# Optimization experiments

Hardware: AMD Instinct MI355X
Metric: run time of the kernel (lower is better)

The kernel has to match this reference:

```python
import jax, jax.numpy as jnp
import numpy as np
from jax import lax

EPS = 1e-5
H = 4      # num_heads
D = 64     # qkv_dim (== in_channels)


def _bn(x, gamma, beta, mean, var):
    # eval-mode BatchNorm2d over NCHW, channel axis 1
    inv = gamma / jnp.sqrt(var + EPS)
    return x * inv[:, None, None] + (beta - mean * inv)[:, None, None]


def _conv(x, w, b, pad_w):
    y = lax.conv_general_dilated(x, w, window_strides=(1, 1),
                                 padding=[(0, 0), (pad_w, pad_w)],
                                 dimension_numbers=("NCHW", "OIHW", "NCHW"))
    return y + b[None, :, None, None]


def setup_inputs() -> dict:
    key = jax.random.key(0)
    ks = jax.random.split(key, 16)
    N, C, T, V = 16, 64, 64, 25
    s = 0.05
    return {
        "x": jax.random.normal(ks[0], (N, C, T, V), jnp.float32),
        "W_qkv": jax.random.normal(ks[1], (C, 3 * H * D), jnp.float32) * s,
        "b_qkv": jax.random.normal(ks[2], (3 * H * D,), jnp.float32) * s,
        "W_out": jax.random.normal(ks[3], (C, C * H, 1, 9), jnp.float32) * s,
        "b_out": jax.random.normal(ks[4], (C,), jnp.float32) * s,
        "bn1_gamma": jax.random.uniform(ks[5], (C,), jnp.float32) + 0.5,
        "bn1_beta": jax.random.normal(ks[6], (C,), jnp.float32) * s,
        "bn1_mean": jax.random.normal(ks[7], (C,), jnp.float32) * s,
        "bn1_var": jax.random.uniform(ks[8], (C,), jnp.float32) + 0.5,
        "W_ff": jax.random.normal(ks[9], (C, C, 1, 1), jnp.float32) * s,
        "b_ff": jax.random.normal(ks[10], (C,), jnp.float32) * s,
        "bn2_gamma": jax.random.uniform(ks[11], (C,), jnp.float32) + 0.5,
        "bn2_beta": jax.random.normal(ks[12], (C,), jnp.float32) * s,
        "bn2_mean": jax.random.normal(ks[13], (C,), jnp.float32) * s,
        "bn2_var": jax.random.uniform(ks[14], (C,), jnp.float32) + 0.5,
    }


def reference(x, W_qkv, b_qkv, W_out, b_out, bn1_gamma, bn1_beta, bn1_mean,
              bn1_var, W_ff, b_ff, bn2_gamma, bn2_beta, bn2_mean, bn2_var):
    N, C, T, V = x.shape
    L = T * V
    # qkv projection on [N,T,V,C]
    xt = jnp.transpose(x, (0, 2, 3, 1))                        # [N,T,V,C]
    qkv = xt.reshape(N, L, C) @ W_qkv + b_qkv                  # [N,L,3*H*D]
    qkv = qkv.reshape(N, L, 3, H, D)
    q = jnp.transpose(qkv[:, :, 0], (0, 2, 1, 3))              # [N,H,L,D]
    k = jnp.transpose(qkv[:, :, 1], (0, 2, 1, 3))              # [N,H,L,D]
    v = jnp.transpose(qkv[:, :, 2], (0, 2, 1, 3))              # [N,H,L,D]
    attn = jnp.einsum("nhld,nhmd->nhlm", q, k) / jnp.sqrt(jnp.float32(D))
    attn = jax.nn.softmax(attn, axis=-1)
    o = jnp.einsum("nhlm,nhmd->nhld", attn, v)                 # [N,H,L,D]
    # view(N,H,T,V,D).permute(0,1,4,2,3).view(N,H*D,T,V)
    o = o.reshape(N, H, T, V, D)
    o = jnp.transpose(o, (0, 1, 4, 2, 3)).reshape(N, H * D, T, V)
    # out_nets: Conv2d (1,9) pad (0,4) + BN, residual (identity), relu
    y = _bn(_conv(o, W_out, b_out, 4), bn1_gamma, bn1_beta, bn1_mean, bn1_var)
    y = jax.nn.relu(y + x)
    # ff_net: 1x1 conv + BN, residual, relu
    z = _bn(_conv(y, W_ff, b_ff, 0), bn2_gamma, bn2_beta, bn2_mean, bn2_var)
    return jax.nn.relu(z + y)
```

## Files before the change

kernel.cpp:

```cpp
#include <hip/hip_runtime.h>
#include <hip/hip_bf16.h>

#define NB 16
#define CC 64
#define TT 64
#define VV 25
#define LL 1600
#define HH 4
#define DD 64
#define NH 64


typedef __hip_bfloat16 bf16;
typedef __attribute__((ext_vector_type(8))) short short8;
typedef __attribute__((ext_vector_type(4))) float f32x4;
typedef __attribute__((ext_vector_type(4))) int int4v;
typedef __attribute__((ext_vector_type(4))) unsigned short us4;

__device__ __forceinline__ float b2f(bf16 v) { return __bfloat162float(v); }
__device__ __forceinline__ unsigned short f2bf_bits(float f) {
  bf16 h = __float2bfloat16(f);
  return *(unsigned short*)&h;
}
__device__ __forceinline__ unsigned pkbf_trunc(float lo, float hi) {
  return __builtin_amdgcn_perm(__float_as_uint(hi), __float_as_uint(lo), 0x07060302u);
}
__device__ __forceinline__ float dppx1(float x) {
  return __int_as_float(
      __builtin_amdgcn_mov_dpp(__float_as_int(x), 0xB1, 0xF, 0xF, true));
}
__device__ __forceinline__ int dppx1i(int x) {
  return __builtin_amdgcn_mov_dpp(x, 0xB1, 0xF, 0xF, true);
}
__device__ __forceinline__ void pl32swap(int &a, int &b) {
  asm("v_permlane32_swap_b32 %0, %1" : "+v"(a), "+v"(b));
}
__device__ __forceinline__ void pl16swap(int &a, int &b) {
  asm("v_permlane16_swap_b32 %0, %1" : "+v"(a), "+v"(b));
}

__global__ void k_prep(const float* __restrict__ Wo, const float* __restrict__ Wf,
                       const float* __restrict__ Wq,
                       bf16* __restrict__ Wt, bf16* __restrict__ WfT,
                       bf16* __restrict__ WqT) {
  int i = blockIdx.x * 256 + threadIdx.x;
  if (i < 147456) {
    int j = i & 7, lane = (i >> 3) & 63, cot = (i >> 9) & 3;
    int kc = (i >> 11) & 7, r = i >> 14;
    int co = cot * 16 + (lane & 15);
    int ci = kc * 32 + (lane >> 4) * 8 + j;
    Wt[i] = __float2bfloat16(Wo[(co * 256 + ci) * 9 + r]);
  }
  if (i < 4096) {
    int j = i & 7, lane = (i >> 3) & 63, cot = (i >> 9) & 3, kc = (i >> 11) & 1;
    int co = cot * 16 + (lane & 15);
    int ci = kc * 32 + (lane >> 4) * 8 + j;
    WfT[i] = __float2bfloat16(Wf[co * 64 + ci]);
  }
  if (i < 49152) {
    int jj = i & 7, lane = (i >> 3) & 63, g = i >> 9;
    int nt = g % 48, half = g / 48;
    int ch = half * 32 + (lane >> 4) * 8 + jj;
    int j = nt * 16 + (lane & 15);
    WqT[i] = __float2bfloat16(Wq[ch * 768 + j]);
  }
}

__global__ __launch_bounds__(64)
void k_qkv(const float* __restrict__ x, const bf16* __restrict__ WqT,
           const float* __restrict__ bq,
           bf16* __restrict__ q, bf16* __restrict__ k, bf16* __restrict__ vt) {
  __shared__ short xa[16 * 72];
  __shared__ short tr[16 * 66];
  int lane = threadIdx.x;
  int quad = lane >> 4, c = lane & 15;
  int n = blockIdx.x / 100;
  int l0 = (blockIdx.x % 100) * 16;
  bool ev = (c & 1) == 0;

  {
    int l = c;
    const float* xb = x + (size_t)n * 102400 + (size_t)(quad * 16) * 1600 + l0 + l;
    unsigned short vb[16];
#pragma unroll
    for (int i = 0; i < 16; i++) vb[i] = f2bf_bits(xb[(size_t)i * 1600]);
    unsigned wrds[8];
#pragma unroll
    for (int i = 0; i < 8; i++)
      wrds[i] = ((unsigned)vb[2 * i + 1] << 16) | vb[2 * i];
    *(short8*)(xa + l * 72 + quad * 16) = *(short8*)&wrds[0];
    *(short8*)(xa + l * 72 + quad * 16 + 8) = *(short8*)&wrds[4];
  }
  asm volatile("" ::: "memory");
  short8 af0 = *(const short8*)(xa + c * 72 + quad * 8);
  short8 af1 = *(const short8*)(xa + c * 72 + 32 + quad * 8);

  const short* wq0 = (const short*)WqT;
  const float QSCALE = 0.125f * 1.44269504f;

  short8 bc[8], bn[8];
#pragma unroll
  for (int t = 0; t < 4; t++) {
    bc[2 * t]     = *(const short8*)(wq0 + ((size_t)t * 64 + lane) * 8);
    bc[2 * t + 1] = *(const short8*)(wq0 + ((size_t)(48 + t) * 64 + lane) * 8);
  }

#pragma unroll
  for (int g = 0; g < 12; g++) {
    int s = g >> 2, h = g & 3;
    f32x4 z[4];
#pragma unroll
    for (int t = 0; t < 4; t++) {
      int nt = g * 4 + t;
      float bv = bq[nt * 16 + c];
      f32x4 zz = {bv, bv, bv, bv};
      zz = __builtin_amdgcn_mfma_f32_16x16x32_bf16(af0, bc[2 * t], zz, 0, 0, 0);
      zz = __builtin_amdgcn_mfma_f32_16x16x32_bf16(af1, bc[2 * t + 1], zz, 0, 0, 0);
      z[t] = zz;
    }
    if (g < 11) {
#pragma unroll
      for (int t = 0; t < 4; t++) {
        int nt = (g + 1) * 4 + t;
        bn[2 * t]     = *(const short8*)(wq0 + ((size_t)nt * 64 + lane) * 8);
        bn[2 * t + 1] = *(const short8*)(wq0 + ((size_t)(48 + nt) * 64 + lane) * 8);
      }
    }
    if (s < 2) {
      asm volatile("" ::: "memory");
#pragma unroll
      for (int t = 0; t < 4; t++) {
        if (s == 0) {
#pragma unroll
          for (int r = 0; r < 4; r++) z[t][r] *= QSCALE;
        }
        int us_[4];
#pragma unroll
        for (int r = 0; r < 4; r++) us_[r] = f2bf_bits(z[t][r]);
        int xv0 = dppx1i(us_[0]);
        int xv1 = dppx1i(us_[1]);
        int xv2 = dppx1i(us_[2]);
        int xv3 = dppx1i(us_[3]);
        if (ev) {
          *(int*)(tr + (quad * 4 + 0) * 66 + t * 16 + c) = (xv0 << 16) | us_[0];
          *(int*)(tr + (quad * 4 + 1) * 66 + t * 16 + c) = (xv1 << 16) | us_[1];
        } else {
          *(int*)(tr + (quad * 4 + 2) * 66 + t * 16 + (c - 1)) = (us_[2] << 16) | xv2;
          *(int*)(tr + (quad * 4 + 3) * 66 + t * 16 + (c - 1)) = (us_[3] << 16) | xv3;
        }
      }
      asm volatile("" ::: "memory");
      int row = lane >> 2, seg = lane & 3;
      short8 o0 = *(const short8*)(tr + row * 66 + seg * 16);
      short8 o1 = *(const short8*)(tr + row * 66 + seg * 16 + 8);
      short* dstp = (short*)(s == 0 ? q : k);
      short* dst = dstp + ((size_t)(n * 4 + h) * 1600 + l0 + row) * 64 + seg * 16;
      *(short8*)(dst) = o0;
      *(short8*)(dst + 8) = o1;
      asm volatile("" ::: "memory");
    } else {
#pragma unroll
      for (int t = 0; t < 4; t++) {
        us4 pk;
#pragma unroll
        for (int r = 0; r < 4; r++) pk[r] = f2bf_bits(z[t][r]);
        *(us4*)((short*)vt + ((size_t)((n * 4 + h) * 64 + t * 16 + c)) * 1600 +
                l0 + quad * 4) = pk;
      }
    }
#pragma unroll
    for (int i = 0; i < 8; i++) bc[i] = bn[i];
  }
}

__global__ __launch_bounds__(128, 2)
void k_attn(const bf16* __restrict__ q, const bf16* __restrict__ k,
            const bf16* __restrict__ vt, bf16* __restrict__ po,
            float* __restrict__ ls, int split) {
  __shared__ short kbuf[64 * 72];
  __shared__ short vbuf[64 * 72];
  __shared__ short pl_all[2][16 * 66];
  int tid = threadIdx.x;
  int wv = tid >> 6, lane = tid & 63;
  int quad = lane >> 4, c = lane & 15;
  int bid = blockIdx.x;
  int xcd = bid & 7;
  int slot = bid >> 3;
  int half, qt, grp;
  if (split == 2) { half = slot & 1; qt = (slot >> 1) % 25; grp = slot / 50; }
  else            { half = 0;        qt = slot % 25;        grp = slot / 25; }
  int nh = grp * 8 + xcd;
  int kt0 = half ? 13 : 0;
  int kt1 = (split == 2 && half == 0) ? 13 : 25;
  int l0 = qt * 64 + wv * 32;
  short* pl = pl_all[wv];

  const short* qbase = (const short*)q + ((size_t)nh * 1600 + l0 + c) * 64 + quad * 8;
  short8 qf[2][2];
  qf[0][0] = *(const short8*)(qbase);
  qf[0][1] = *(const short8*)(qbase + 32);
  qf[1][0] = *(const short8*)(qbase + 16 * 64);
  qf[1][1] = *(const short8*)(qbase + 16 * 64 + 32);

  short ob = (c == 0) ? (short)0x3F80 : (short)0;
  short8 onesf = {ob, ob, ob, ob, ob, ob, ob, ob};

  f32x4 acc[2][5] = {};

  const short* kg = (const short*)k + (size_t)nh * 102400;
  const short* vg = (const short*)vt + (size_t)nh * 102400;
  bool ev = (c & 1) == 0;

  short8 sk[4], sv[4];
  {
    const short8* gk = (const short8*)(kg + kt0 * 4096);
#pragma unroll
    for (int i = 0; i < 4; i++) sk[i] = gk[tid + i * 128];
#pragma unroll
    for (int i = 0; i < 4; i++) {
      int ch = tid + i * 128;
      sv[i] = *(const short8*)(vg + (size_t)(ch >> 3) * 1600 + kt0 * 64 + (ch & 7) * 8);
    }
  }

  for (int kt = kt0; kt < kt1; kt++) {
    __syncthreads();
#pragma unroll
    for (int i = 0; i < 4; i++) {
      int ch = tid + i * 128;
      *(short8*)(kbuf + (ch >> 3) * 72 + (ch & 7) * 8) = sk[i];
      *(short8*)(vbuf + (ch >> 3) * 72 + (ch & 7) * 8) = sv[i];
    }
    __syncthreads();
    if (kt + 1 < kt1) {
      const short8* gk = (const short8*)(kg + (kt + 1) * 4096);
#pragma unroll
      for (int i = 0; i < 4; i++) sk[i] = gk[tid + i * 128];
#pragma unroll
      for (int i = 0; i < 4; i++) {
        int ch = tid + i * 128;
        sv[i] = *(const short8*)(vg + (size_t)(ch >> 3) * 1600 + (kt + 1) * 64 + (ch & 7) * 8);
      }
    }
    f32x4 s[2][4];
#pragma unroll
    for (int ct = 0; ct < 4; ct++) {
      short8 kf0 = *(const short8*)(kbuf + (ct * 16 + c) * 72 + quad * 8);
      short8 kf1 = *(const short8*)(kbuf + (ct * 16 + c) * 72 + 32 + quad * 8);
      f32x4 z0 = {-8.f, -8.f, -8.f, -8.f}, z1 = {-8.f, -8.f, -8.f, -8.f};
      z0 = __builtin_amdgcn_mfma_f32_16x16x32_bf16(kf0, qf[0][0], z0, 0, 0, 0);
      z0 = __builtin_amdgcn_mfma_f32_16x16x32_bf16(kf1, qf[0][1], z0, 0, 0, 0);
      z1 = __builtin_amdgcn_mfma_f32_16x16x32_bf16(kf0, qf[1][0], z1, 0, 0, 0);
      z1 = __builtin_amdgcn_mfma_f32_16x16x32_bf16(kf1, qf[1][1], z1, 0, 0, 0);
      s[0][ct] = z0;
      s[1][ct] = z1;
    }
#pragma unroll
    for (int tt = 0; tt < 2; tt++)
#pragma unroll
      for (int ct = 0; ct < 4; ct++)
#pragma unroll
        for (int r = 0; r < 4; r++) s[tt][ct][r] = exp2f(s[tt][ct][r]);
    short8 vf[4][2];
#pragma unroll
    for (int ct = 0; ct < 4; ct++) {
      vf[ct][0] = *(const short8*)(vbuf + (ct * 16 + c) * 72 + quad * 8);
      vf[ct][1] = *(const short8*)(vbuf + (ct * 16 + c) * 72 + 32 + quad * 8);
    }
#pragma unroll
    for (int tt = 0; tt < 2; tt++) {
      int wA[4], wB[4];
#pragma unroll
      for (int ct = 0; ct < 4; ct++) {
        wA[ct] = (int)pkbf_trunc(s[tt][ct][0], s[tt][ct][1]);
        wB[ct] = (int)pkbf_trunc(s[tt][ct][2], s[tt][ct][3]);
      }
      pl32swap(wA[0], wA[1]); pl16swap(wA[0], wA[1]);
      pl32swap(wB[0], wB[1]); pl16swap(wB[0], wB[1]);
      int4v f0 = {wA[0], wB[0], wA[1], wB[1]};
      pl32swap(wA[2], wA[3]); pl16swap(wA[2], wA[3]);
      pl32swap(wB[2], wB[3]); pl16swap(wB[2], wB[3]);
      int4v f1 = {wA[2], wB[2], wA[3], wB[3]};
      short8 pf0 = *(short8*)&f0;
      short8 pf1 = *(short8*)&f1;
#pragma unroll
      for (int ct = 0; ct < 4; ct++) {
        acc[tt][ct] = __builtin_amdgcn_mfma_f32_16x16x32_bf16(pf0, vf[ct][0], acc[tt][ct], 0, 0, 0);
        acc[tt][ct] = __builtin_amdgcn_mfma_f32_16x16x32_bf16(pf1, vf[ct][1], acc[tt][ct], 0, 0, 0);
      }
      acc[tt][4] = __builtin_amdgcn_mfma_f32_16x16x32_bf16(pf0, onesf, acc[tt][4], 0, 0, 0);
      acc[tt][4] = __builtin_amdgcn_mfma_f32_16x16x32_bf16(pf1, onesf, acc[tt][4], 0, 0, 0);
    }
  }
  int n = nh >> 2, h = nh & 3;
#pragma unroll
  for (int tt = 0; tt < 2; tt++) {
    float linv[4] = {1.f, 1.f, 1.f, 1.f};
    if (split == 1) {
#pragma unroll
      for (int r = 0; r < 4; r++)
        linv[r] = 1.0f / __shfl(acc[tt][4][r], lane & 48);
    }
    asm volatile("" ::: "memory");
#pragma unroll
    for (int t = 0; t < 4; t++) {
      int us_[4];
#pragma unroll
      for (int r = 0; r < 4; r++) us_[r] = f2bf_bits(acc[tt][t][r] * linv[r]);
      int xv0 = dppx1i(us_[0]);
      int xv1 = dppx1i(us_[1]);
      int xv2 = dppx1i(us_[2]);
      int xv3 = dppx1i(us_[3]);
      if (ev) {
        *(int*)(pl + (quad * 4 + 0) * 66 + t * 16 + c) = (xv0 << 16) | us_[0];
        *(int*)(pl + (quad * 4 + 1) * 66 + t * 16 + c) = (xv1 << 16) | us_[1];
      } else {
        *(int*)(pl + (quad * 4 + 2) * 66 + t * 16 + (c - 1)) = (us_[2] << 16) | xv2;
        *(int*)(pl + (quad * 4 + 3) * 66 + t * 16 + (c - 1)) = (us_[3] << 16) | xv3;
      }
    }
    asm volatile("" ::: "memory");
    int row = lane >> 2, seg = lane & 3;
    short8 o0 = *(const short8*)(pl + row * 66 + seg * 16);
    short8 o1 = *(const short8*)(pl + row * 66 + seg * 16 + 8);
    short* dst = (short*)po + (size_t)half * 6553600 +
                 ((size_t)n * 1600 + l0 + tt * 16 + row) * 256 + h * 64 + seg * 16;
    *(short8*)(dst) = o0;
    *(short8*)(dst + 8) = o1;
    if (split == 2 && c == 0) {
#pragma unroll
      for (int r = 0; r < 4; r++)
        ls[half * 102400 + nh * 1600 + l0 + tt * 16 + quad * 4 + r] = acc[tt][4][r];
    }
    asm volatile("" ::: "memory");
  }
}

__global__ void k_comb(const bf16* po_in, const float* __restrict__ ls, bf16* ot) {
  int i = blockIdx.x * 256 + threadIdx.x;
  int ch8 = i & 31;
  int rest = i >> 5;
  int l = rest % 1600;
  int n = rest / 1600;
  int nh = n * 4 + (ch8 >> 3);
  float inv = 1.0f / (ls[nh * 1600 + l] + ls[102400 + nh * 1600 + l]);
  const short* a = (const short*)po_in + (size_t)rest * 256 + ch8 * 8;
  short8 av = *(const short8*)a;
  short8 bv = *(const short8*)(a + 6553600);
  unsigned short o8[8];
#pragma unroll
  for (int j = 0; j < 8; j++) {
    float fa = __uint_as_float(((unsigned)(unsigned short)av[j]) << 16);
    float fb = __uint_as_float(((unsigned)(unsigned short)bv[j]) << 16);
    o8[j] = f2bf_bits((fa + fb) * inv);
  }
  *(short8*)((short*)ot + (size_t)rest * 256 + ch8 * 8) = *(short8*)o8;
}

__global__ void k_conv9(const bf16* __restrict__ ot, const bf16* __restrict__ Wt,
                        const float* __restrict__ bo, const float* __restrict__ g1,
                        const float* __restrict__ be1, const float* __restrict__ mu1,
                        const float* __restrict__ va1, const float* __restrict__ x,
                        const bf16* __restrict__ WfT, const float* __restrict__ bff,
                        const float* __restrict__ g2, const float* __restrict__ be2,
                        const float* __restrict__ mu2, const float* __restrict__ va2,
                        float* __restrict__ out) {
  __shared__ short tl[2][16 * 66];
  int wv = threadIdx.x >> 6;
  int lane = threadIdx.x & 63;
  int quad = lane >> 4, c = lane & 15;
  int n = blockIdx.y;
  int l0 = blockIdx.x * 32 + wv * 16;
  int la = l0 + c;
  int va = la % 25;
  const short* obase = (const short*)ot + (size_t)n * 409600;
  const short* wbase = (const short*)Wt;
  f32x4 acc[4] = {};
  for (int r = 0; r < 9; r++) {
    int sh = r - 4;
    bool valid = (unsigned)(va + sh) < 25u;
    int lp = la + sh;
    lp = max(0, min(1599, lp));
    const short* arow = obase + (size_t)lp * 256 + quad * 8;
    const short* wrow = wbase + (size_t)r * 8 * 4 * 64 * 8 + lane * 8;
    short8 z8 = {0, 0, 0, 0, 0, 0, 0, 0};
#pragma unroll 4
    for (int kc = 0; kc < 8; kc++) {
      short8 af = *(const short8*)(arow + kc * 32);
      af = valid ? af : z8;
      const short* wk = wrow + kc * 4 * 64 * 8;
      short8 b0 = *(const short8*)(wk);
      short8 b1 = *(const short8*)(wk + 512);
      short8 b2 = *(const short8*)(wk + 1024);
      short8 b3 = *(const short8*)(wk + 1536);
      acc[0] = __builtin_amdgcn_mfma_f32_16x16x32_bf16(af, b0, acc[0], 0, 0, 0);
      acc[1] = __builtin_amdgcn_mfma_f32_16x16x32_bf16(af, b1, acc[1], 0, 0, 0);
      acc[2] = __builtin_amdgcn_mfma_f32_16x16x32_bf16(af, b2, acc[2], 0, 0, 0);
      acc[3] = __builtin_amdgcn_mfma_f32_16x16x32_bf16(af, b3, acc[3], 0, 0, 0);
    }
  }
  short* tlw = &tl[wv][0];
  float outv[4][4];
#pragma unroll
  for (int cot = 0; cot < 4; cot++) {
    int co = cot * 16 + c;
    float inv = g1[co] * rsqrtf(va1[co] + 1e-5f);
    float add = be1[co] - mu1[co] * inv + bo[co] * inv;
    f32x4 xr = *(const f32x4*)(x + (size_t)(n * 64 + co) * 1600 + l0 + quad * 4);
#pragma unroll
    for (int rr = 0; rr < 4; rr++)
      outv[cot][rr] = fmaxf(acc[cot][rr] * inv + add + xr[rr], 0.f);
  }
  asm volatile("" ::: "memory");
  bool ev = (c & 1) == 0;
#pragma unroll
  for (int cot = 0; cot < 4; cot++) {
    int us_[4];
#pragma unroll
    for (int rr = 0; rr < 4; rr++) us_[rr] = f2bf_bits(outv[cot][rr]);
    int xv0 = dppx1i(us_[0]);
    int xv1 = dppx1i(us_[1]);
    int xv2 = dppx1i(us_[2]);
    int xv3 = dppx1i(us_[3]);
    if (ev) {
      *(int*)(tlw + (quad * 4 + 0) * 66 + cot * 16 + c) = (xv0 << 16) | us_[0];
      *(int*)(tlw + (quad * 4 + 1) * 66 + cot * 16 + c) = (xv1 << 16) | us_[1];
    } else {
      *(int*)(tlw + (quad * 4 + 2) * 66 + cot * 16 + (c - 1)) = (us_[2] << 16) | xv2;
      *(int*)(tlw + (quad * 4 + 3) * 66 + cot * 16 + (c - 1)) = (us_[3] << 16) | xv3;
    }
  }
  asm volatile("" ::: "memory");
  short8 afY0 = *(const short8*)(tlw + c * 66 + quad * 8);
  short8 afY1 = *(const short8*)(tlw + c * 66 + 32 + quad * 8);
  const short* wfb = (const short*)WfT + lane * 8;
  f32x4 acc2[4] = {};
#pragma unroll
  for (int kc = 0; kc < 2; kc++) {
    short8 afk = kc ? afY1 : afY0;
    const short* wk = wfb + kc * 2048;
    short8 b0 = *(const short8*)(wk);
    short8 b1 = *(const short8*)(wk + 512);
    short8 b2 = *(const short8*)(wk + 1024);
    short8 b3 = *(const short8*)(wk + 1536);
    acc2[0] = __builtin_amdgcn_mfma_f32_16x16x32_bf16(afk, b0, acc2[0], 0, 0, 0);
    acc2[1] = __builtin_amdgcn_mfma_f32_16x16x32_bf16(afk, b1, acc2[1], 0, 0, 0);
    acc2[2] = __builtin_amdgcn_mfma_f32_16x16x32_bf16(afk, b2, acc2[2], 0, 0, 0);
    acc2[3] = __builtin_amdgcn_mfma_f32_16x16x32_bf16(afk, b3, acc2[3], 0, 0, 0);
  }
#pragma unroll
  for (int cot = 0; cot < 4; cot++) {
    int co = cot * 16 + c;
    float inv = g2[co] * rsqrtf(va2[co] + 1e-5f);
    float add = be2[co] - mu2[co] * inv + bff[co] * inv;
    f32x4 ov;
#pragma unroll
    for (int rr = 0; rr < 4; rr++)
      ov[rr] = fmaxf(acc2[cot][rr] * inv + add + outv[cot][rr], 0.f);
    *(f32x4*)(out + (size_t)(n * 64 + co) * 1600 + l0 + quad * 4) = ov;
  }
}

extern "C" void kernel_launch(void* const* d_in, const int* in_sizes, int n_in,
                              void* d_out, int out_size, void* d_ws, size_t ws_size,
                              hipStream_t stream) {
  const float* x   = (const float*)d_in[0];
  const float* Wq  = (const float*)d_in[1];
  const float* bq  = (const float*)d_in[2];
  const float* Wo  = (const float*)d_in[3];
  const float* bo  = (const float*)d_in[4];
  const float* g1  = (const float*)d_in[5];
  const float* be1 = (const float*)d_in[6];
  const float* mu1 = (const float*)d_in[7];
  const float* va1 = (const float*)d_in[8];
  const float* Wf  = (const float*)d_in[9];
  const float* bff = (const float*)d_in[10];
  const float* g2  = (const float*)d_in[11];
  const float* be2 = (const float*)d_in[12];
  const float* mu2 = (const float*)d_in[13];
  const float* va2 = (const float*)d_in[14];

  const size_t QKV = (size_t)64 * 1600 * 64;
  size_t elems2 = 5 * QKV + 147456 + 4096 + 49152;
  size_t need2 = elems2 * 2 + 2 * 102400 * 4 + 256;
  int split = (ws_size >= need2) ? 2 : 1;

  bf16* qw  = (bf16*)d_ws;
  bf16* kw  = qw + QKV;
  bf16* vtw = kw + QKV;
  bf16* pow_ = vtw + QKV;
  bf16* Wt  = pow_ + (size_t)split * QKV;
  bf16* WfT = Wt + 147456;
  bf16* WqT = WfT + 4096;
  float* ls = (float*)(WqT + 49152);

  k_prep<<<576, 256, 0, stream>>>(Wo, Wf, Wq, Wt, WfT, WqT);
  k_qkv<<<1600, 64, 0, stream>>>(x, WqT, bq, qw, kw, vtw);
  k_attn<<<split * 1600, 128, 0, stream>>>(qw, kw, vtw, pow_, ls, split);
  if (split == 2) k_comb<<<3200, 256, 0, stream>>>(pow_, ls, pow_);
  dim3 gc(50, 16);
  k_conv9<<<gc, 128, 0, stream>>>(pow_, Wt, bo, g1, be1, mu1, va1, x,
                                  WfT, bff, g2, be2, mu2, va2, (float*)d_out);
}
```

Measured before the change: 229.0 us.

## Double-buffer K/V tiles in LDS to drop one barrier per iteration

The attention kernel now keeps two LDS buffers each for K and V. While the current tile is consumed from one buffer, the next tile (already held in registers) is stored into the other, and the tile after that is prefetched from global memory. This cuts the two __syncthreads per key tile to one and lets LDS stores overlap with MFMA work. In exchange, LDS use per block doubles and one redundant global prefetch is issued on the last iteration.

Result: slower. 244.6 us (+6.8%).

```diff
diff --git a/kernel.cpp b/kernel.cpp
--- a/kernel.cpp
+++ b/kernel.cpp
@@ -177,8 +177,8 @@
 void k_attn(const bf16* __restrict__ q, const bf16* __restrict__ k,
             const bf16* __restrict__ vt, bf16* __restrict__ po,
             float* __restrict__ ls, int split) {
-  __shared__ short kbuf[64 * 72];
-  __shared__ short vbuf[64 * 72];
+  __shared__ short kbuf[2][64 * 72];
+  __shared__ short vbuf[2][64 * 72];
   __shared__ short pl_all[2][16 * 66];
   int tid = threadIdx.x;
   int wv = tid >> 6, lane = tid & 63;
@@ -221,32 +221,52 @@
       int ch = tid + i * 128;
       sv[i] = *(const short8*)(vg + (size_t)(ch >> 3) * 1600 + kt0 * 64 + (ch & 7) * 8);
     }
-  }
-
-  for (int kt = kt0; kt < kt1; kt++) {
-    __syncthreads();
 #pragma unroll
     for (int i = 0; i < 4; i++) {
       int ch = tid + i * 128;
-      *(short8*)(kbuf + (ch >> 3) * 72 + (ch & 7) * 8) = sk[i];
-      *(short8*)(vbuf + (ch >> 3) * 72 + (ch & 7) * 8) = sv[i];
-    }
-    __syncthreads();
-    if (kt + 1 < kt1) {
-      const short8* gk = (const short8*)(kg + (kt + 1) * 4096);
+      *(short8*)(kbuf[0] + (ch >> 3) * 72 + (ch & 7) * 8) = sk[i];
+      *(short8*)(vbuf[0] + (ch >> 3) * 72 + (ch & 7) * 8) = sv[i];
+    }
+    int ktp = kt0 + 1;
+    const short8* gk1 = (const short8*)(kg + ktp * 4096);
+#pragma unroll
+    for (int i = 0; i < 4; i++) sk[i] = gk1[tid + i * 128];
+#pragma unroll
+    for (int i = 0; i < 4; i++) {
+      int ch = tid + i * 128;
+      sv[i] = *(const short8*)(vg + (size_t)(ch >> 3) * 1600 + ktp * 64 + (ch & 7) * 8);
+    }
+  }
+  __syncthreads();
+  int cur = 0;
+
+  for (int kt = kt0; kt < kt1; kt++) {
+    short* kb = kbuf[cur];
+    short* vb = vbuf[cur];
+    short* kbn = kbuf[cur ^ 1];
+    short* vbn = vbuf[cur ^ 1];
+#pragma unroll
+    for (int i = 0; i < 4; i++) {
+      int ch = tid + i * 128;
+      *(short8*)(kbn + (ch >> 3) * 72 + (ch & 7) * 8) = sk[i];
+      *(short8*)(vbn + (ch >> 3) * 72 + (ch & 7) * 8) = sv[i];
+    }
+    {
+      int ktn = (kt + 2 < kt1) ? (kt + 2) : kt0;
+      const short8* gk = (const short8*)(kg + ktn * 4096);
 #pragma unroll
       for (int i = 0; i < 4; i++) sk[i] = gk[tid + i * 128];
 #pragma unroll
       for (int i = 0; i < 4; i++) {
         int ch = tid + i * 128;
-        sv[i] = *(const short8*)(vg + (size_t)(ch >> 3) * 1600 + (kt + 1) * 64 + (ch & 7) * 8);
+        sv[i] = *(const short8*)(vg + (size_t)(ch >> 3) * 1600 + ktn * 64 + (ch & 7) * 8);
       }
     }
     f32x4 s[2][4];
 #pragma unroll
     for (int ct = 0; ct < 4; ct++) {
-      short8 kf0 = *(const short8*)(kbuf + (ct * 16 + c) * 72 + quad * 8);
-      short8 kf1 = *(const short8*)(kbuf + (ct * 16 + c) * 72 + 32 + quad * 8);
+      short8 kf0 = *(const short8*)(kb + (ct * 16 + c) * 72 + quad * 8);
+      short8 kf1 = *(const short8*)(kb + (ct * 16 + c) * 72 + 32 + quad * 8);
       f32x4 z0 = {-8.f, -8.f, -8.f, -8.f}, z1 = {-8.f, -8.f, -8.f, -8.f};
       z0 = __builtin_amdgcn_mfma_f32_16x16x32_bf16(kf0, qf[0][0], z0, 0, 0, 0);
       z0 = __builtin_amdgcn_mfma_f32_16x16x32_bf16(kf1, qf[0][1], z0, 0, 0, 0);
@@ -264,8 +284,8 @@
     short8 vf[4][2];
 #pragma unroll
     for (int ct = 0; ct < 4; ct++) {
-      vf[ct][0] = *(const short8*)(vbuf + (ct * 16 + c) * 72 + quad * 8);
-      vf[ct][1] = *(const short8*)(vbuf + (ct * 16 + c) * 72 + 32 + quad * 8);
+      vf[ct][0] = *(const short8*)(vb + (ct * 16 + c) * 72 + quad * 8);
+      vf[ct][1] = *(const short8*)(vb + (ct * 16 + c) * 72 + 32 + quad * 8);
     }
 #pragma unroll
     for (int tt = 0; tt < 2; tt++) {
@@ -291,6 +311,8 @@
       acc[tt][4] = __builtin_amdgcn_mfma_f32_16x16x32_bf16(pf0, onesf, acc[tt][4], 0, 0, 0);
       acc[tt][4] = __builtin_amdgcn_mfma_f32_16x16x32_bf16(pf1, onesf, acc[tt][4], 0, 0, 0);
     }
+    __syncthreads();
+    cur ^= 1;
   }
   int n = nh >> 2, h = nh & 3;
 #pragma unroll
```

## Split attention query tile across four waves of sixteen rows each

Applied to the files above, without the earlier changes.

Each attention block now runs four waves instead of two. Each wave handles 16 query rows instead of 32, so the 64-row query tile per block stays the same. The K/V staging load per thread halves, and per-wave register use (accumulators, score tiles) drops, which should allow more waves in flight per CU. In exchange, each K/V fragment read from LDS now feeds half as many MFMAs, which raises LDS traffic relative to compute, and more threads take part in each barrier.

Measured after the change: 222.1 us. 1.03x faster.

```diff
diff --git a/kernel.cpp b/kernel.cpp
--- a/kernel.cpp
+++ b/kernel.cpp
@@ -173,13 +173,13 @@
   }
 }
 
-__global__ __launch_bounds__(128, 2)
+__global__ __launch_bounds__(256, 2)
 void k_attn(const bf16* __restrict__ q, const bf16* __restrict__ k,
             const bf16* __restrict__ vt, bf16* __restrict__ po,
             float* __restrict__ ls, int split) {
   __shared__ short kbuf[64 * 72];
   __shared__ short vbuf[64 * 72];
-  __shared__ short pl_all[2][16 * 66];
+  __shared__ short pl_all[4][16 * 66];
   int tid = threadIdx.x;
   int wv = tid >> 6, lane = tid & 63;
   int quad = lane >> 4, c = lane & 15;
@@ -192,33 +192,30 @@
   int nh = grp * 8 + xcd;
   int kt0 = half ? 13 : 0;
   int kt1 = (split == 2 && half == 0) ? 13 : 25;
-  int l0 = qt * 64 + wv * 32;
+  int l0 = qt * 64 + wv * 16;
   short* pl = pl_all[wv];
 
   const short* qbase = (const short*)q + ((size_t)nh * 1600 + l0 + c) * 64 + quad * 8;
-  short8 qf[2][2];
-  qf[0][0] = *(const short8*)(qbase);
-  qf[0][1] = *(const short8*)(qbase + 32);
-  qf[1][0] = *(const short8*)(qbase + 16 * 64);
-  qf[1][1] = *(const short8*)(qbase + 16 * 64 + 32);
+  short8 qf0 = *(const short8*)(qbase);
+  short8 qf1 = *(const short8*)(qbase + 32);
 
   short ob = (c == 0) ? (short)0x3F80 : (short)0;
   short8 onesf = {ob, ob, ob, ob, ob, ob, ob, ob};
 
-  f32x4 acc[2][5] = {};
+  f32x4 acc[5] = {};
 
   const short* kg = (const short*)k + (size_t)nh * 102400;
   const short* vg = (const short*)vt + (size_t)nh * 102400;
   bool ev = (c & 1) == 0;
 
-  short8 sk[4], sv[4];
+  short8 sk[2], sv[2];
   {
     const short8* gk = (const short8*)(kg + kt0 * 4096);
 #pragma unroll
-    for (int i = 0; i < 4; i++) sk[i] = gk[tid + i * 128];
-#pragma unroll
-    for (int i = 0; i < 4; i++) {
-      int ch = tid + i * 128;
+    for (int i = 0; i < 2; i++) sk[i] = gk[tid + i * 256];
+#pragma unroll
+    for (int i = 0; i < 2; i++) {
+      int ch = tid + i * 256;
       sv[i] = *(const short8*)(vg + (size_t)(ch >> 3) * 1600 + kt0 * 64 + (ch & 7) * 8);
     }
   }
@@ -226,8 +223,8 @@
   for (int kt = kt0; kt < kt1; kt++) {
     __syncthreads();
 #pragma unroll
-    for (int i = 0; i < 4; i++) {
-      int ch = tid + i * 128;
+    for (int i = 0; i < 2; i++) {
+      int ch = tid + i * 256;
       *(short8*)(kbuf + (ch >> 3) * 72 + (ch & 7) * 8) = sk[i];
       *(short8*)(vbuf + (ch >> 3) * 72 + (ch & 7) * 8) = sv[i];
     }
@@ -235,45 +232,39 @@
     if (kt + 1 < kt1) {
       const short8* gk = (const short8*)(kg + (kt + 1) * 4096);
 #pragma unroll
-      for (int i = 0; i < 4; i++) sk[i] = gk[tid + i * 128];
-#pragma unroll
-      for (int i = 0; i < 4; i++) {
-        int ch = tid + i * 128;
+      for (int i = 0; i < 2; i++) sk[i] = gk[tid + i * 256];
+#pragma unroll
+      for (int i = 0; i < 2; i++) {
+        int ch = tid + i * 256;
         sv[i] = *(const short8*)(vg + (size_t)(ch >> 3) * 1600 + (kt + 1) * 64 + (ch & 7) * 8);
       }
     }
-    f32x4 s[2][4];
+    f32x4 s[4];
 #pragma unroll
     for (int ct = 0; ct < 4; ct++) {
       short8 kf0 = *(const short8*)(kbuf + (ct * 16 + c) * 72 + quad * 8);
       short8 kf1 = *(const short8*)(kbuf + (ct * 16 + c) * 72 + 32 + quad * 8);
-      f32x4 z0 = {-8.f, -8.f, -8.f, -8.f}, z1 = {-8.f, -8.f, -8.f, -8.f};
-      z0 = __builtin_amdgcn_mfma_f32_16x16x32_bf16(kf0, qf[0][0], z0, 0, 0, 0);
-      z0 = __builtin_amdgcn_mfma_f32_16x16x32_bf16(kf1, qf[0][1], z0, 0, 0, 0);
-      z1 = __builtin_amdgcn_mfma_f32_16x16x32_bf16(kf0, qf[1][0], z1, 0, 0, 0);
-      z1 = __builtin_amdgcn_mfma_f32_16x16x32_bf16(kf1, qf[1][1], z1, 0, 0, 0);
-      s[0][ct] = z0;
-      s[1][ct] = z1;
-    }
-#pragma unroll
-    for (int tt = 0; tt < 2; tt++)
-#pragma unroll
-      for (int ct = 0; ct < 4; ct++)
-#pragma unroll
-        for (int r = 0; r < 4; r++) s[tt][ct][r] = exp2f(s[tt][ct][r]);
+      f32x4 z0 = {-8.f, -8.f, -8.f, -8.f};
+      z0 = __builtin_amdgcn_mfma_f32_16x16x32_bf16(kf0, qf0, z0, 0, 0, 0);
+      z0 = __builtin_amdgcn_mfma_f32_16x16x32_bf16(kf1, qf1, z0, 0, 0, 0);
+      s[ct] = z0;
+    }
+#pragma unroll
+    for (int ct = 0; ct < 4; ct++)
+#pragma unroll
+      for (int r = 0; r < 4; r++) s[ct][r] = exp2f(s[ct][r]);
     short8 vf[4][2];
 #pragma unroll
     for (int ct = 0; ct < 4; ct++) {
       vf[ct][0] = *(const short8*)(vbuf + (ct * 16 + c) * 72 + quad * 8);
       vf[ct][1] = *(const short8*)(vbuf + (ct * 16 + c) * 72 + 32 + quad * 8);
     }
-#pragma unroll
-    for (int tt = 0; tt < 2; tt++) {
+    {
       int wA[4], wB[4];
 #pragma unroll
       for (int ct = 0; ct < 4; ct++) {
-        wA[ct] = (int)pkbf_trunc(s[tt][ct][0], s[tt][ct][1]);
-        wB[ct] = (int)pkbf_trunc(s[tt][ct][2], s[tt][ct][3]);
+        wA[ct] = (int)pkbf_trunc(s[ct][0], s[ct][1]);
+        wB[ct] = (int)pkbf_trunc(s[ct][2], s[ct][3]);
       }
       pl32swap(wA[0], wA[1]); pl16swap(wA[0], wA[1]);
       pl32swap(wB[0], wB[1]); pl16swap(wB[0], wB[1]);
@@ -285,28 +276,27 @@
       short8 pf1 = *(short8*)&f1;
 #pragma unroll
       for (int ct = 0; ct < 4; ct++) {
-        acc[tt][ct] = __builtin_amdgcn_mfma_f32_16x16x32_bf16(pf0, vf[ct][0], acc[tt][ct], 0, 0, 0);
-        acc[tt][ct] = __builtin_amdgcn_mfma_f32_16x16x32_bf16(pf1, vf[ct][1], acc[tt][ct], 0, 0, 0);
-      }
-      acc[tt][4] = __builtin_amdgcn_mfma_f32_16x16x32_bf16(pf0, onesf, acc[tt][4], 0, 0, 0);
-      acc[tt][4] = __builtin_amdgcn_mfma_f32_16x16x32_bf16(pf1, onesf, acc[tt][4], 0, 0, 0);
+        acc[ct] = __builtin_amdgcn_mfma_f32_16x16x32_bf16(pf0, vf[ct][0], acc[ct], 0, 0, 0);
+        acc[ct] = __builtin_amdgcn_mfma_f32_16x16x32_bf16(pf1, vf[ct][1], acc[ct], 0, 0, 0);
+      }
+      acc[4] = __builtin_amdgcn_mfma_f32_16x16x32_bf16(pf0, onesf, acc[4], 0, 0, 0);
+      acc[4] = __builtin_amdgcn_mfma_f32_16x16x32_bf16(pf1, onesf, acc[4], 0, 0, 0);
     }
   }
   int n = nh >> 2, h = nh & 3;
-#pragma unroll
-  for (int tt = 0; tt < 2; tt++) {
+  {
     float linv[4] = {1.f, 1.f, 1.f, 1.f};
     if (split == 1) {
 #pragma unroll
       for (int r = 0; r < 4; r++)
-        linv[r] = 1.0f / __shfl(acc[tt][4][r], lane & 48);
+        linv[r] = 1.0f / __shfl(acc[4][r], lane & 48);
     }
     asm volatile("" ::: "memory");
 #pragma unroll
     for (int t = 0; t < 4; t++) {
       int us_[4];
 #pragma unroll
-      for (int r = 0; r < 4; r++) us_[r] = f2bf_bits(acc[tt][t][r] * linv[r]);
+      for (int r = 0; r < 4; r++) us_[r] = f2bf_bits(acc[t][r] * linv[r]);
       int xv0 = dppx1i(us_[0]);
       int xv1 = dppx1i(us_[1]);
       int xv2 = dppx1i(us_[2]);
@@ -324,13 +314,13 @@
     short8 o0 = *(const short8*)(pl + row * 66 + seg * 16);
     short8 o1 = *(const short8*)(pl + row * 66 + seg * 16 + 8);
     short* dst = (short*)po + (size_t)half * 6553600 +
-                 ((size_t)n * 1600 + l0 + tt * 16 + row) * 256 + h * 64 + seg * 16;
+                 ((size_t)n * 1600 + l0 + row) * 256 + h * 64 + seg * 16;
     *(short8*)(dst) = o0;
     *(short8*)(dst + 8) = o1;
     if (split == 2 && c == 0) {
 #pragma unroll
       for (int r = 0; r < 4; r++)
-        ls[half * 102400 + nh * 1600 + l0 + tt * 16 + quad * 4 + r] = acc[tt][4][r];
+        ls[half * 102400 + nh * 1600 + l0 + quad * 4 + r] = acc[4][r];
     }
     asm volatile("" ::: "memory");
   }
@@ -496,7 +486,7 @@
 
   k_prep<<<576, 256, 0, stream>>>(Wo, Wf, Wq, Wt, WfT, WqT);
   k_qkv<<<1600, 64, 0, stream>>>(x, WqT, bq, qw, kw, vtw);
-  k_attn<<<split * 1600, 128, 0, stream>>>(qw, kw, vtw, pow_, ls, split);
+  k_attn<<<split * 1600, 256, 0, stream>>>(qw, kw, vtw, pow_, ls, split);
   if (split == 2) k_comb<<<3200, 256, 0, stream>>>(pow_, ls, pow_);
   dim3 gc(50, 16);
   k_conv9<<<gc, 128, 0, stream>>>(pow_, Wt, bo, g1, be1, mu1, va1, x,
```
